# Kernel optimization log

Measured on AMD Instinct MI355X. Metric: run time of the kernel, lower is better.

## Reference

```python
import math
import jax, jax.numpy as jnp
import numpy as np

N_HEAD = 16

def setup_inputs() -> dict:
    key = jax.random.key(0)
    ks = jax.random.split(key, 7)
    B, T, C = 4, 2048, 1024
    QL, KVL = 256, 256
    s = 0.02
    return {
        "x":     jax.random.normal(ks[0], (B, T, C), jnp.float32),
        "W_dq":  jax.random.normal(ks[1], (QL, C), jnp.float32) * s,
        "W_uq":  jax.random.normal(ks[2], (C, QL), jnp.float32) * s,
        "W_dkv": jax.random.normal(ks[3], (KVL, C), jnp.float32) * s,
        "W_uk":  jax.random.normal(ks[4], (C, KVL), jnp.float32) * s,
        "W_uv":  jax.random.normal(ks[5], (C, KVL), jnp.float32) * s,
        "W_o":   jax.random.normal(ks[6], (C, C), jnp.float32) * s,
    }

def reference(x, W_dq, W_uq, W_dkv, W_uk, W_uv, W_o):
    B, T, C = x.shape
    nh = N_HEAD
    hs = C // nh
    kvl = W_dkv.shape[0]
    # Absorbed projection matrices (training path: recomputed each call)
    # k_eff: (nh, hs, kvl); v_eff: (nh, kvl, hs)
    k_eff = (W_dq.T @ W_uq.T @ W_uk).reshape(nh, hs, kvl)
    v_eff = (W_uv.T @ W_o.T).reshape(kvl, nh, hs).transpose(1, 0, 2)
    # Latent KV cache: (B, T, kvl)
    c_kv = x @ W_dkv.T
    # Queries: (B, nh, T, hs)
    q = (x @ W_dq.T @ W_uq.T).reshape(B, T, nh, hs).transpose(0, 2, 1, 3)
    # Scores: q @ k_eff @ c_kv^T / sqrt(hs) -> (B, nh, T, T)
    q_lat = jnp.einsum('bhtd,hdl->bhtl', q, k_eff)
    attn = jnp.einsum('bhtl,bsl->bhts', q_lat, c_kv) / math.sqrt(hs)
    causal_mask = jnp.triu(jnp.ones((T, T), bool), k=1)
    attn = jnp.where(causal_mask[None, None], -jnp.inf, attn)
    attn = jax.nn.softmax(attn, axis=-1)  # dropout p=0 -> identity
    # Output: attn @ c_kv @ v_eff -> (B, T, C)
    ctx = jnp.einsum('bhts,bsl->bhtl', attn, c_kv)
    y = jnp.einsum('bhtl,hld->bhtd', ctx, v_eff).transpose(0, 2, 1, 3).reshape(B, T, C)
    return (y, c_kv)
```

## Files before the change

### kernel.cpp

```cpp
#include <hip/hip_runtime.h>

typedef unsigned short u16;
typedef __attribute__((ext_vector_type(8))) short short8;
typedef __attribute__((ext_vector_type(4))) float f32x4;

#define MFMA_BF16 __builtin_amdgcn_mfma_f32_16x16x32_bf16

__device__ __forceinline__ u16 f2bf(float f){
  unsigned int u = __builtin_bit_cast(unsigned int, f);
  u += 0x7fffu + ((u >> 16) & 1u);
  return (u16)(u >> 16);
}

__device__ __forceinline__ void gld16(const void* g, void* l){
  __builtin_amdgcn_global_load_lds(
      (const __attribute__((address_space(1))) unsigned int*)g,
      (__attribute__((address_space(3))) unsigned int*)l, 16, 0, 0);
}

__global__ void k_transpose4(const float* __restrict__ s0, float* __restrict__ d0,
                             const float* __restrict__ s1, float* __restrict__ d1,
                             const float* __restrict__ s2, float* __restrict__ d2,
                             const float* __restrict__ s3, float* __restrict__ d3)
{
  __shared__ float tile[32][33];
  int z = blockIdx.z;
  const float* src = z == 0 ? s0 : z == 1 ? s1 : z == 2 ? s2 : s3;
  float* dst       = z == 0 ? d0 : z == 1 ? d1 : z == 2 ? d2 : d3;
  int rows = z == 0 ? 256 : 1024, cols = z == 0 ? 1024 : 256;
  int c0 = blockIdx.x * 32, r0 = blockIdx.y * 32;
  if (c0 >= cols || r0 >= rows) return;
  int tx = threadIdx.x, ty = threadIdx.y;
#pragma unroll
  for (int i = 0; i < 4; ++i){
    int r = ty + i * 8;
    tile[r][tx] = src[(long)(r0 + r) * cols + c0 + tx];
  }
  __syncthreads();
#pragma unroll
  for (int i = 0; i < 4; ++i){
    int r = ty + i * 8;
    dst[(long)(c0 + r) * rows + r0 + tx] = tile[tx][r];
  }
}

__global__ __launch_bounds__(256)
void k_gemm_nt(const float* __restrict__ A, const float* __restrict__ B,
               float* __restrict__ Cf, u16* __restrict__ Cb,
               int M, int N, int K, int lda, int ldb, int ldc,
               long sA, long sB, long sC, float scale)
{
  A += (long)blockIdx.z * sA; B += (long)blockIdx.z * sB;
  if (Cf) Cf += (long)blockIdx.z * sC;
  if (Cb) Cb += (long)blockIdx.z * sC;
  const int n0 = blockIdx.x * 64, m0 = blockIdx.y * 64;
  const int tid = threadIdx.x;
  const int wave = tid >> 6, lane = tid & 63, quad = lane >> 4, l16 = lane & 15;
  __shared__ u16 As[64 * 40];
  __shared__ u16 Bs[64 * 40];
  f32x4 acc[4];
#pragma unroll
  for (int n = 0; n < 4; ++n) acc[n] = (f32x4){0.f, 0.f, 0.f, 0.f};

  const int lr = tid >> 2;
  const int lc = (tid & 3) * 8;
  for (int k0 = 0; k0 < K; k0 += 32){
    {
      const float* pa = &A[(long)(m0 + lr) * lda + k0 + lc];
      float4 a0 = *(const float4*)pa;
      float4 a1 = *(const float4*)(pa + 4);
      short8 pk;
      pk[0]=(short)f2bf(a0.x); pk[1]=(short)f2bf(a0.y); pk[2]=(short)f2bf(a0.z); pk[3]=(short)f2bf(a0.w);
      pk[4]=(short)f2bf(a1.x); pk[5]=(short)f2bf(a1.y); pk[6]=(short)f2bf(a1.z); pk[7]=(short)f2bf(a1.w);
      *(short8*)&As[lr * 40 + lc] = pk;
      const float* pb = &B[(long)(n0 + lr) * ldb + k0 + lc];
      float4 b0 = *(const float4*)pb;
      float4 b1 = *(const float4*)(pb + 4);
      short8 qk;
      qk[0]=(short)f2bf(b0.x); qk[1]=(short)f2bf(b0.y); qk[2]=(short)f2bf(b0.z); qk[3]=(short)f2bf(b0.w);
      qk[4]=(short)f2bf(b1.x); qk[5]=(short)f2bf(b1.y); qk[6]=(short)f2bf(b1.z); qk[7]=(short)f2bf(b1.w);
      *(short8*)&Bs[lr * 40 + lc] = qk;
    }
    __syncthreads();
    short8 a = *(const short8*)&As[(wave * 16 + l16) * 40 + quad * 8];
#pragma unroll
    for (int n = 0; n < 4; ++n){
      short8 b = *(const short8*)&Bs[(n * 16 + l16) * 40 + quad * 8];
      acc[n] = MFMA_BF16(a, b, acc[n], 0, 0, 0);
    }
    __syncthreads();
  }
#pragma unroll
  for (int n = 0; n < 4; ++n)
#pragma unroll
    for (int r = 0; r < 4; ++r){
      int row = m0 + wave * 16 + quad * 4 + r;
      int col = n0 + n * 16 + l16;
      float v = acc[n][r] * scale;
      if (Cf) Cf[(long)row * ldc + col] = v;
      if (Cb) Cb[(long)row * ldc + col] = f2bf(v);
    }
}

__global__ __launch_bounds__(256)
void k_proj(const float* __restrict__ x, const float* __restrict__ Wdq,
            const float* __restrict__ Wdkv, u16* __restrict__ xq,
            float* __restrict__ ckv_f, u16* __restrict__ ckv_bf, u16* __restrict__ ckvT)
{
  const bool is_kv = blockIdx.x >= 4;
  const float* B = is_kv ? Wdkv : Wdq;
  const int n0 = (blockIdx.x & 3) * 64, m0 = blockIdx.y * 64;
  const int tid = threadIdx.x;
  const int wave = tid >> 6, lane = tid & 63, quad = lane >> 4, l16 = lane & 15;
  __shared__ u16 As[64 * 40];
  __shared__ u16 Bs[64 * 40];
  f32x4 acc[4];
#pragma unroll
  for (int n = 0; n < 4; ++n) acc[n] = (f32x4){0.f, 0.f, 0.f, 0.f};

  const int lr = tid >> 2;
  const int lc = (tid & 3) * 8;
  for (int k0 = 0; k0 < 1024; k0 += 32){
    {
      const float* pa = &x[(long)(m0 + lr) * 1024 + k0 + lc];
      float4 a0 = *(const float4*)pa;
      float4 a1 = *(const float4*)(pa + 4);
      short8 pk;
      pk[0]=(short)f2bf(a0.x); pk[1]=(short)f2bf(a0.y); pk[2]=(short)f2bf(a0.z); pk[3]=(short)f2bf(a0.w);
      pk[4]=(short)f2bf(a1.x); pk[5]=(short)f2bf(a1.y); pk[6]=(short)f2bf(a1.z); pk[7]=(short)f2bf(a1.w);
      *(short8*)&As[lr * 40 + lc] = pk;
      const float* pb = &B[(long)(n0 + lr) * 1024 + k0 + lc];
      float4 b0 = *(const float4*)pb;
      float4 b1 = *(const float4*)(pb + 4);
      short8 qk;
      qk[0]=(short)f2bf(b0.x); qk[1]=(short)f2bf(b0.y); qk[2]=(short)f2bf(b0.z); qk[3]=(short)f2bf(b0.w);
      qk[4]=(short)f2bf(b1.x); qk[5]=(short)f2bf(b1.y); qk[6]=(short)f2bf(b1.z); qk[7]=(short)f2bf(b1.w);
      *(short8*)&Bs[lr * 40 + lc] = qk;
    }
    __syncthreads();
    short8 a = *(const short8*)&As[(wave * 16 + l16) * 40 + quad * 8];
#pragma unroll
    for (int n = 0; n < 4; ++n){
      short8 b = *(const short8*)&Bs[(n * 16 + l16) * 40 + quad * 8];
      acc[n] = MFMA_BF16(a, b, acc[n], 0, 0, 0);
    }
    __syncthreads();
  }
  if (!is_kv){
#pragma unroll
    for (int n = 0; n < 4; ++n)
#pragma unroll
      for (int r = 0; r < 4; ++r){
        int row = m0 + wave * 16 + quad * 4 + r;
        int col = n0 + n * 16 + l16;
        xq[(long)row * 256 + col] = f2bf(acc[n][r]);
      }
  } else {
    const int b = (m0 >> 11);
    const int t0 = (m0 & 2047) + wave * 16 + quad * 4;
#pragma unroll
    for (int n = 0; n < 4; ++n){
      int col = n0 + n * 16 + l16;
      u16 pk[4];
#pragma unroll
      for (int r = 0; r < 4; ++r){
        int row = m0 + wave * 16 + quad * 4 + r;
        float v = acc[n][r];
        ckv_f [(long)row * 256 + col] = v;
        ckv_bf[(long)row * 256 + col] = f2bf(v);
        pk[r] = f2bf(v);
      }
      *(uint2*)&ckvT[((long)b * 256 + col) * 2048 + t0] = *(uint2*)pk;
    }
  }
}

__global__ __launch_bounds__(512, 2)
void k_flash(const u16* __restrict__ xq, const u16* __restrict__ Pt,
             const u16* __restrict__ ckv_bf, const u16* __restrict__ ckvT,
             const u16* __restrict__ Vt, float* __restrict__ y)
{
  const int qt = 15 - blockIdx.x, h = blockIdx.y, b = blockIdx.z;
  const int tid = threadIdx.x;
  const int wg = tid >> 6, lane = tid & 63, quad = lane >> 4, l16 = lane & 15;

  __shared__ u16 LDS[40960];
  u16* X0 = LDS;
  u16* X1 = LDS + 16384;
  u16* PW = LDS + 32768 + wg * 1024;

  const int trow = wg * 16 + l16;
  const int swr  = l16 & 7;
  const long tglob = (long)b * 2048 + qt * 128;

  const u16* ckv_b  = ckv_bf + (long)b * 2048 * 256;
  const u16* ckvT_b = ckvT   + (long)b * 256 * 2048;

  int offA[4], offB[4];
  {
    int l5 = lane >> 5, g32 = lane & 31;
#pragma unroll
    for (int j = 0; j < 4; ++j){
      int s = (wg * 4 + j) * 2 + l5;
      offA[j] = s * 256 + ((g32 ^ (s & 7)) * 8);
    }
    int l3 = lane >> 3, g8 = lane & 7;
#pragma unroll
    for (int j = 0; j < 4; ++j){
      int l = (wg * 4 + j) * 8 + l3;
      offB[j] = l * 2048 + ((g8 ^ (l & 7)) * 8);
    }
  }

  short8 aS[8];
  {
    short8 bq[8];
    const u16* xr = xq + (tglob + trow) * 256;
#pragma unroll
    for (int ks = 0; ks < 8; ++ks)
      bq[ks] = *(const short8*)&xr[ks * 32 + quad * 8];
    const u16* pth = Pt + (long)h * 65536;
#pragma unroll
    for (int mb = 0; mb < 16; ++mb){
      f32x4 acc = (f32x4){0.f, 0.f, 0.f, 0.f};
#pragma unroll
      for (int ks = 0; ks < 8; ++ks){
        short8 pa = *(const short8*)&pth[(mb * 16 + l16) * 256 + ks * 32 + quad * 8];
        acc = MFMA_BF16(pa, bq[ks], acc, 0, 0, 0);
      }
#pragma unroll
      for (int r = 0; r < 4; ++r){
        int l = mb * 16 + quad * 4 + r;
        int cs = (((l >> 3) ^ swr) << 3) | (l & 7);
        LDS[trow * 256 + cs] = f2bf(acc[r]);
      }
    }
  }
  __syncthreads();
#pragma unroll
  for (int ks = 0; ks < 8; ++ks){
    int gl = ks * 4 + quad;
    aS[ks] = *(const short8*)&LDS[trow * 256 + ((gl ^ swr) << 3)];
  }

  float m_t = -1e30f, l_t = 0.f;
  f32x4 oacc[16];
#pragma unroll
  for (int n = 0; n < 16; ++n) oacc[n] = (f32x4){0.f, 0.f, 0.f, 0.f};

  const int stmax = 2 * qt + 1;
  const int tg = qt * 128 + trow;
  for (int st = 0; st <= stmax; ++st){
    __syncthreads();
#pragma unroll
    for (int j = 0; j < 4; ++j)
      gld16(ckv_b + (long)st * 16384 + offA[j], &LDS[(wg * 4 + j) * 512]);
#pragma unroll
    for (int j = 0; j < 4; ++j)
      gld16(ckvT_b + st * 64 + offB[j], &LDS[16384 + (wg * 4 + j) * 512]);
    __syncthreads();

    if (st * 64 > qt * 128 + wg * 16 + 15) continue;

    f32x4 sacc[4];
#pragma unroll
    for (int mb = 0; mb < 4; ++mb) sacc[mb] = (f32x4){0.f, 0.f, 0.f, 0.f};
    __builtin_amdgcn_s_setprio(1);
#pragma unroll
    for (int ks = 0; ks < 8; ++ks){
      int gl = ks * 4 + quad;
#pragma unroll
      for (int mb = 0; mb < 4; ++mb){
        short8 a = *(const short8*)&X0[(mb * 16 + l16) * 256 + ((gl ^ swr) << 3)];
        sacc[mb] = MFMA_BF16(a, aS[ks], sacc[mb], 0, 0, 0);
      }
    }
    __builtin_amdgcn_s_setprio(0);

    if (st * 64 + 63 > tg){
#pragma unroll
      for (int mb = 0; mb < 4; ++mb)
#pragma unroll
        for (int r = 0; r < 4; ++r)
          if (st * 64 + mb * 16 + quad * 4 + r > tg) sacc[mb][r] = -1e30f;
    }

    float rm = sacc[0][0];
#pragma unroll
    for (int mb = 0; mb < 4; ++mb)
#pragma unroll
      for (int r = 0; r < 4; ++r) rm = fmaxf(rm, sacc[mb][r]);
    rm = fmaxf(rm, __shfl_xor(rm, 16, 64));
    rm = fmaxf(rm, __shfl_xor(rm, 32, 64));
    if (!__all(rm <= m_t + 8.f)){
      float mnew = fmaxf(m_t, rm);
      float alpha = __expf(m_t - mnew);
      m_t = mnew;
      l_t *= alpha;
#pragma unroll
      for (int r2 = 0; r2 < 4; ++r2){
        float ar = __shfl(alpha, quad * 4 + r2, 64);
#pragma unroll
        for (int n = 0; n < 16; ++n) oacc[n][r2] *= ar;
      }
    }
    float rs = 0.f;
#pragma unroll
    for (int mb = 0; mb < 4; ++mb){
      float p0 = __expf(sacc[mb][0] - m_t);
      float p1 = __expf(sacc[mb][1] - m_t);
      float p2 = __expf(sacc[mb][2] - m_t);
      float p3 = __expf(sacc[mb][3] - m_t);
      rs += (p0 + p1) + (p2 + p3);
      unsigned int w0 = (unsigned)f2bf(p0) | ((unsigned)f2bf(p1) << 16);
      unsigned int w1 = (unsigned)f2bf(p2) | ((unsigned)f2bf(p3) << 16);
      int pos = (2 * mb + (quad >> 1)) ^ swr;
      uint2 w; w.x = w0; w.y = w1;
      *(uint2*)&PW[l16 * 64 + pos * 8 + (quad & 1) * 4] = w;
    }
    rs += __shfl_xor(rs, 16, 64);
    rs += __shfl_xor(rs, 32, 64);
    l_t += rs;

    short8 a0 = *(const short8*)&PW[l16 * 64 + ((quad ^ swr) << 3)];
    short8 a1 = *(const short8*)&PW[l16 * 64 + (((4 + quad) ^ swr) << 3)];
    __builtin_amdgcn_s_setprio(1);
#pragma unroll
    for (int n = 0; n < 16; ++n){
      int lr_ = n * 16 + l16;
      int swl = lr_ & 7;
      short8 b0 = *(const short8*)&X1[lr_ * 64 + ((quad ^ swl) << 3)];
      short8 b1 = *(const short8*)&X1[lr_ * 64 + (((4 + quad) ^ swl) << 3)];
      oacc[n] = MFMA_BF16(a0, b0, oacc[n], 0, 0, 0);
      oacc[n] = MFMA_BF16(a1, b1, oacc[n], 0, 0, 0);
    }
    __builtin_amdgcn_s_setprio(0);
  }

  __syncthreads();
  {
    float linv = 1.f / l_t;
#pragma unroll
    for (int r = 0; r < 4; ++r){
      float lr_ = __shfl(linv, quad * 4 + r, 64);
#pragma unroll
      for (int n = 0; n < 16; ++n) oacc[n][r] *= lr_;
    }
#pragma unroll
    for (int n = 0; n < 16; ++n)
#pragma unroll
      for (int r = 0; r < 4; ++r){
        int trw = wg * 16 + quad * 4 + r;
        int l = n * 16 + l16;
        int cs = (((l >> 3) ^ (trw & 7)) << 3) | (l & 7);
        LDS[trw * 256 + cs] = f2bf(oacc[n][r]);
      }
  }
  __syncthreads();
  {
    const u16* vth = Vt + (long)h * 64 * 256;
    short8 ca[8];
#pragma unroll
    for (int ks = 0; ks < 8; ++ks){
      int gl = ks * 4 + quad;
      ca[ks] = *(const short8*)&LDS[trow * 256 + ((gl ^ swr) << 3)];
    }
#pragma unroll
    for (int n = 0; n < 4; ++n){
      f32x4 acc = (f32x4){0.f, 0.f, 0.f, 0.f};
#pragma unroll
      for (int ks = 0; ks < 8; ++ks){
        short8 vb = *(const short8*)&vth[(n * 16 + l16) * 256 + ks * 32 + quad * 8];
        acc = MFMA_BF16(ca[ks], vb, acc, 0, 0, 0);
      }
#pragma unroll
      for (int r = 0; r < 4; ++r)
        y[(tglob + wg * 16 + quad * 4 + r) * 1024 + h * 64 + n * 16 + l16] = acc[r];
    }
  }
}

extern "C" void kernel_launch(void* const* d_in, const int* in_sizes, int n_in,
                              void* d_out, int out_size, void* d_ws, size_t ws_size,
                              hipStream_t stream)
{
  (void)in_sizes; (void)n_in; (void)out_size; (void)ws_size;
  const float* x    = (const float*)d_in[0];
  const float* Wdq  = (const float*)d_in[1];
  const float* Wuq  = (const float*)d_in[2];
  const float* Wdkv = (const float*)d_in[3];
  const float* Wuk  = (const float*)d_in[4];
  const float* Wuv  = (const float*)d_in[5];
  const float* Wo   = (const float*)d_in[6];

  float* y_out   = (float*)d_out;
  float* ckv_out = y_out + (size_t)4 * 2048 * 1024;

  char* base = (char*)d_ws;
  float* wdqT   = (float*)(base + 0);
  float* wuqT   = (float*)(base + 1048576);
  float* wukT   = (float*)(base + 2097152);
  float* wuvT   = (float*)(base + 3145728);
  u16*   ckvT   = (u16*)  (base + 0);
  float* t1T    = (float*)(base + 4194304);
  float* keffT  = (float*)(base + 4456448);
  u16*   pt     = (u16*)  (base + 5505024);
  u16*   vt     = (u16*)  (base + 7602176);
  u16*   xq     = (u16*)  (base + 8126464);
  u16*   ckv_bf = (u16*)  (base + 12320768);

  k_transpose4<<<dim3(32, 32, 4), dim3(32, 8), 0, stream>>>(
      Wdq, wdqT, Wuq, wuqT, Wuk, wukT, Wuv, wuvT);

  k_gemm_nt<<<dim3(4, 4, 1), 256, 0, stream>>>(wukT, wuqT, t1T, (u16*)0,
      256, 256, 1024, 1024, 1024, 256, 0, 0, 0, 1.f);
  k_gemm_nt<<<dim3(16, 4, 1), 256, 0, stream>>>(t1T, wdqT, keffT, (u16*)0,
      256, 1024, 256, 256, 256, 1024, 0, 0, 0, 1.f);
  k_gemm_nt<<<dim3(4, 4, 16), 256, 0, stream>>>(keffT, wuqT, (float*)0, pt,
      256, 256, 64, 1024, 1024, 256, 64, 64, 65536, 0.125f);
  k_gemm_nt<<<dim3(4, 16, 1), 256, 0, stream>>>(Wo, wuvT, (float*)0, vt,
      1024, 256, 1024, 1024, 1024, 256, 0, 0, 0, 1.f);

  k_proj<<<dim3(8, 128), 256, 0, stream>>>(x, Wdq, Wdkv, xq, ckv_out, ckv_bf, ckvT);

  k_flash<<<dim3(16, 16, 4), 512, 0, stream>>>(xq, pt, ckv_bf, ckvT, vt, y_out);
}
```

Measured before the change: 761.8 us.

## Double-buffer KV tiles with prefetch and halve the KV tile width

The flash loop moves from a load-then-compute scheme with two barriers per 64-wide KV tile to a double-buffered scheme with 32-wide tiles. The next tile's global-to-LDS copy is issued before computing on the current one, leaving one barrier per iteration. The aim is to hide load latency behind the QK and PV MFMAs. The cost is twice as many iterations, so per-tile softmax, shuffle and rescale overhead roughly doubles, and the async LDS loads must be complete by the next barrier.

```diff
diff --git a/kernel.cpp b/kernel.cpp
--- a/kernel.cpp
+++ b/kernel.cpp
@@ -184,31 +184,30 @@
   const int tid = threadIdx.x;
   const int wg = tid >> 6, lane = tid & 63, quad = lane >> 4, l16 = lane & 15;
 
-  __shared__ u16 LDS[40960];
-  u16* X0 = LDS;
-  u16* X1 = LDS + 16384;
-  u16* PW = LDS + 32768 + wg * 1024;
+  __shared__ u16 LDS[36864];
+  u16* PW = LDS + 32768 + wg * 512;
 
   const int trow = wg * 16 + l16;
   const int swr  = l16 & 7;
+  const int swp  = l16 & 3;
   const long tglob = (long)b * 2048 + qt * 128;
 
   const u16* ckv_b  = ckv_bf + (long)b * 2048 * 256;
   const u16* ckvT_b = ckvT   + (long)b * 256 * 2048;
 
-  int offA[4], offB[4];
+  int offA[2], offB[2];
   {
     int l5 = lane >> 5, g32 = lane & 31;
 #pragma unroll
-    for (int j = 0; j < 4; ++j){
-      int s = (wg * 4 + j) * 2 + l5;
+    for (int j = 0; j < 2; ++j){
+      int s = (wg * 2 + j) * 2 + l5;
       offA[j] = s * 256 + ((g32 ^ (s & 7)) * 8);
     }
-    int l3 = lane >> 3, g8 = lane & 7;
-#pragma unroll
-    for (int j = 0; j < 4; ++j){
-      int l = (wg * 4 + j) * 8 + l3;
-      offB[j] = l * 2048 + ((g8 ^ (l & 7)) * 8);
+    int l3 = lane >> 2, g4 = lane & 3;
+#pragma unroll
+    for (int j = 0; j < 2; ++j){
+      int l = (wg * 2 + j) * 16 + l3;
+      offB[j] = l * 2048 + ((g4 ^ (l & 3)) * 8);
     }
   }
 
@@ -242,52 +241,67 @@
     int gl = ks * 4 + quad;
     aS[ks] = *(const short8*)&LDS[trow * 256 + ((gl ^ swr) << 3)];
   }
+  __syncthreads();
+
+#pragma unroll
+  for (int j = 0; j < 2; ++j)
+    gld16(ckv_b + offA[j], &LDS[(wg * 2 + j) * 512]);
+#pragma unroll
+  for (int j = 0; j < 2; ++j)
+    gld16(ckvT_b + offB[j], &LDS[16384 + (wg * 2 + j) * 512]);
 
   float m_t = -1e30f, l_t = 0.f;
   f32x4 oacc[16];
 #pragma unroll
   for (int n = 0; n < 16; ++n) oacc[n] = (f32x4){0.f, 0.f, 0.f, 0.f};
 
-  const int stmax = 2 * qt + 1;
+  const int stmax = 4 * qt + 3;
   const int tg = qt * 128 + trow;
   for (int st = 0; st <= stmax; ++st){
+    const int cur = st & 1;
     __syncthreads();
-#pragma unroll
-    for (int j = 0; j < 4; ++j)
-      gld16(ckv_b + (long)st * 16384 + offA[j], &LDS[(wg * 4 + j) * 512]);
-#pragma unroll
-    for (int j = 0; j < 4; ++j)
-      gld16(ckvT_b + st * 64 + offB[j], &LDS[16384 + (wg * 4 + j) * 512]);
-    __syncthreads();
-
-    if (st * 64 > qt * 128 + wg * 16 + 15) continue;
-
-    f32x4 sacc[4];
-#pragma unroll
-    for (int mb = 0; mb < 4; ++mb) sacc[mb] = (f32x4){0.f, 0.f, 0.f, 0.f};
+    if (st < stmax){
+      const int nx = cur ^ 1;
+#pragma unroll
+      for (int j = 0; j < 2; ++j)
+        gld16(ckv_b + (long)(st + 1) * 8192 + offA[j],
+              &LDS[nx * 8192 + (wg * 2 + j) * 512]);
+#pragma unroll
+      for (int j = 0; j < 2; ++j)
+        gld16(ckvT_b + (st + 1) * 32 + offB[j],
+              &LDS[16384 + nx * 8192 + (wg * 2 + j) * 512]);
+    }
+    if (st * 32 > qt * 128 + wg * 16 + 15) continue;
+
+    const u16* X0 = LDS + cur * 8192;
+    const u16* X1 = LDS + 16384 + cur * 8192;
+
+    f32x4 sacc[2];
+#pragma unroll
+    for (int mb = 0; mb < 2; ++mb) sacc[mb] = (f32x4){0.f, 0.f, 0.f, 0.f};
     __builtin_amdgcn_s_setprio(1);
 #pragma unroll
     for (int ks = 0; ks < 8; ++ks){
       int gl = ks * 4 + quad;
 #pragma unroll
-      for (int mb = 0; mb < 4; ++mb){
+      for (int mb = 0; mb < 2; ++mb){
         short8 a = *(const short8*)&X0[(mb * 16 + l16) * 256 + ((gl ^ swr) << 3)];
         sacc[mb] = MFMA_BF16(a, aS[ks], sacc[mb], 0, 0, 0);
       }
     }
     __builtin_amdgcn_s_setprio(0);
 
-    if (st * 64 + 63 > tg){
-#pragma unroll
-      for (int mb = 0; mb < 4; ++mb)
+    if (st * 32 + 31 > tg){
+#pragma unroll
+      for (int mb = 0; mb < 2; ++mb)
 #pragma unroll
         for (int r = 0; r < 4; ++r)
-          if (st * 64 + mb * 16 + quad * 4 + r > tg) sacc[mb][r] = -1e30f;
+          if (st * 32 + mb * 16 + quad * 4 + r > tg) sacc[mb][r] = -1e30f;
     }
 
     float rm = sacc[0][0];
 #pragma unroll
-    for (int mb = 0; mb < 4; ++mb)
+    for (int mb = 0; mb < 2; ++mb)
 #pragma unroll
       for (int r = 0; r < 4; ++r) rm = fmaxf(rm, sacc[mb][r]);
     rm = fmaxf(rm, __shfl_xor(rm, 16, 64));
@@ -306,7 +320,7 @@
     }
     float rs = 0.f;
 #pragma unroll
-    for (int mb = 0; mb < 4; ++mb){
+    for (int mb = 0; mb < 2; ++mb){
       float p0 = __expf(sacc[mb][0] - m_t);
       float p1 = __expf(sacc[mb][1] - m_t);
       float p2 = __expf(sacc[mb][2] - m_t);
@@ -314,25 +328,22 @@
       rs += (p0 + p1) + (p2 + p3);
       unsigned int w0 = (unsigned)f2bf(p0) | ((unsigned)f2bf(p1) << 16);
       unsigned int w1 = (unsigned)f2bf(p2) | ((unsigned)f2bf(p3) << 16);
-      int pos = (2 * mb + (quad >> 1)) ^ swr;
+      int pos = (2 * mb + (quad >> 1)) ^ swp;
       uint2 w; w.x = w0; w.y = w1;
-      *(uint2*)&PW[l16 * 64 + pos * 8 + (quad & 1) * 4] = w;
+      *(uint2*)&PW[l16 * 32 + pos * 8 + (quad & 1) * 4] = w;
     }
     rs += __shfl_xor(rs, 16, 64);
     rs += __shfl_xor(rs, 32, 64);
     l_t += rs;
 
-    short8 a0 = *(const short8*)&PW[l16 * 64 + ((quad ^ swr) << 3)];
-    short8 a1 = *(const short8*)&PW[l16 * 64 + (((4 + quad) ^ swr) << 3)];
+    short8 a0 = *(const short8*)&PW[l16 * 32 + ((quad ^ swp) << 3)];
     __builtin_amdgcn_s_setprio(1);
 #pragma unroll
     for (int n = 0; n < 16; ++n){
       int lr_ = n * 16 + l16;
-      int swl = lr_ & 7;
-      short8 b0 = *(const short8*)&X1[lr_ * 64 + ((quad ^ swl) << 3)];
-      short8 b1 = *(const short8*)&X1[lr_ * 64 + (((4 + quad) ^ swl) << 3)];
+      int swl = lr_ & 3;
+      short8 b0 = *(const short8*)&X1[lr_ * 32 + ((quad ^ swl) << 3)];
       oacc[n] = MFMA_BF16(a0, b0, oacc[n], 0, 0, 0);
-      oacc[n] = MFMA_BF16(a1, b1, oacc[n], 0, 0, 0);
     }
     __builtin_amdgcn_s_setprio(0);
   }
```

New measurement: 760.1 us. Within noise of the previous version (-0.2%).
